# Kernel optimization log

Hardware: AMD Instinct MI355X
Metric: run time of the kernel (lower is better)

## Reference

```python
import jax, jax.numpy as jnp
import numpy as np

G = 250          # grid_size hardcoded in forward
CENTER = G // 2  # 125
K = 1000         # max steps of torch.linspace(r, 2, int((2-r)*500)+1) for r in (0,1)
PAD = 1          # kernel_size // 2 for kernel_size=3
PRED = 10


def rasterize(lidar):
    """Vectorized polar_to_cartesian: lidar [B,360] -> binary grid [B,1,G,G]."""
    B = lidar.shape[0]
    dtype = lidar.dtype
    angles = jnp.linspace(0.0, 2.0 * jnp.pi, 360)            # [360]
    r = lidar                                                 # [B,360]
    valid_r = (r > 0.0) & (r < 1.0)
    # steps = int((2-r)*500) + 1  (positive -> floor == trunc)
    n = jnp.floor((2.0 - r) * 500.0).astype(jnp.int32) + 1   # [B,360], in [501,1000]
    k = jnp.arange(K, dtype=jnp.int32)                        # [K]
    denom = jnp.maximum(n - 1, 1).astype(dtype)
    # torch.linspace(r, 2, n): mag_k = r + k*(2-r)/(n-1)
    mag = r[..., None] + k.astype(dtype) * (2.0 - r)[..., None] / denom[..., None]  # [B,360,K]
    step_ok = k[None, None, :] < n[..., None]
    x = mag * jnp.cos(angles)[None, :, None]
    y = mag * jnp.sin(angles)[None, :, None]
    # int(.) truncates toward zero
    xg = jnp.trunc(CENTER + x * 100.0).astype(jnp.int32)
    yg = jnp.trunc(CENTER + y * 100.0).astype(jnp.int32)
    inb = (xg >= 0) & (xg < G) & (yg >= 0) & (yg < G)
    valid = valid_r[..., None] & step_ok & inb               # [B,360,K]
    idx = jnp.where(valid, yg * G + xg, G * G)               # invalid -> sentinel slot
    flat = jnp.zeros((B, G * G + 1), dtype=dtype)
    flat = flat.at[jnp.arange(B)[:, None, None], idx].max(valid.astype(dtype))
    return flat[:, : G * G].reshape(B, 1, G, G)


def conv2d(x, w, b):
    y = jax.lax.conv_general_dilated(
        x, w, window_strides=(1, 1), padding=[(PAD, PAD), (PAD, PAD)],
        dimension_numbers=("NCHW", "OIHW", "NCHW"))
    return y + b[None, :, None, None]


def linear(x, w, b):  # torch convention: w [out,in]
    return x @ w.T + b


def setup_inputs() -> dict:
    key = jax.random.key(0)
    ks = jax.random.split(key, 18)
    B = 8
    HW, HL = 64, 64  # hidden_size_wind, hidden_size_lidar
    conv_out = 32 * G * G  # 2,000,000

    def w(k, shape, fan_in):
        return jax.random.normal(k, shape, dtype=jnp.float32) / np.float32(np.sqrt(fan_in))

    return {
        "lidar": jax.random.uniform(ks[0], (B, 360), dtype=jnp.float32),
        "wind": jax.random.normal(ks[1], (B, 2), dtype=jnp.float32),
        "w_wind1": w(ks[2], (HW, 2), 2), "b_wind1": jnp.zeros((HW,), jnp.float32),
        "w_wind2": w(ks[3], (HW, HW), HW), "b_wind2": jnp.zeros((HW,), jnp.float32),
        "w_wind3": w(ks[4], (HW, HW), HW), "b_wind3": jnp.zeros((HW,), jnp.float32),
        "conv1_w": w(ks[5], (16, 1, 3, 3), 9), "conv1_b": jnp.zeros((16,), jnp.float32),
        "conv2_w": w(ks[6], (32, 16, 3, 3), 16 * 9), "conv2_b": jnp.zeros((32,), jnp.float32),
        "fc1_w": w(ks[7], (HL, conv_out + HW), conv_out + HW), "fc1_b": jnp.zeros((HL,), jnp.float32),
        "fc2_w": w(ks[8], (HL // 2, HL), HL), "fc2_b": jnp.zeros((HL // 2,), jnp.float32),
        "fc3_w": w(ks[9], (2 * PRED * PRED, HL // 2), HL // 2), "fc3_b": jnp.zeros((2 * PRED * PRED,), jnp.float32),
    }


def reference(lidar, wind, w_wind1, b_wind1, w_wind2, b_wind2, w_wind3, b_wind3,
              conv1_w, conv1_b, conv2_w, conv2_b, fc1_w, fc1_b, fc2_w, fc2_b, fc3_w, fc3_b):
    B = lidar.shape[0]
    img = rasterize(lidar)                                    # [B,1,250,250]
    wnd = jax.nn.relu(linear(wind, w_wind1, b_wind1))
    wnd = jax.nn.relu(linear(wnd, w_wind2, b_wind2))
    wnd = jax.nn.relu(linear(wnd, w_wind3, b_wind3))          # [B,64]
    h = jax.nn.relu(conv2d(img, conv1_w, conv1_b))            # [B,16,250,250]
    h = jax.nn.relu(conv2d(h, conv2_w, conv2_b))              # [B,32,250,250]
    h = h.reshape(B, -1)                                      # [B,2000000]
    x = jnp.concatenate([h, wnd], axis=1)
    x = jax.nn.relu(linear(x, fc1_w, fc1_b))
    x = jax.nn.relu(linear(x, fc2_w, fc2_b))
    x = linear(x, fc3_w, fc3_b)
    return x.reshape(B, PRED, PRED, 2)
```

## Files before the change

### kernel.cpp

```cpp
#include <hip/hip_runtime.h>

#define G 250
#define GG 62500
#define NB 8
#define HFEAT 2000000
#define W1STRIDE 2000064

__global__ void k_raster(const float* __restrict__ lidar, float* __restrict__ img) {
    int idx = blockIdx.x * blockDim.x + threadIdx.x;
    if (idx >= NB * 360 * 1000) return;
    int k = idx % 1000;
    int ba = idx / 1000;
    int a = ba % 360;
    int b = ba / 360;
    float r = lidar[ba];
    if (!(r > 0.0f && r < 1.0f)) return;
    float tmr = __fsub_rn(2.0f, r);
    int n = (int)floorf(__fmul_rn(tmr, 500.0f)) + 1;
    if (k >= n) return;
    float denom = (float)(n - 1);
    const float delta = 6.2831855f / 359.0f;
    float angle = __fmul_rn((float)a, delta);
    float mag = __fadd_rn(r, __fdiv_rn(__fmul_rn((float)k, tmr), denom));
    float c = cosf(angle);
    float s = sinf(angle);
    float px = __fadd_rn(125.0f, __fmul_rn(__fmul_rn(mag, c), 100.0f));
    float py = __fadd_rn(125.0f, __fmul_rn(__fmul_rn(mag, s), 100.0f));
    int xg = (int)px;
    int yg = (int)py;
    if (xg >= 0 && xg < G && yg >= 0 && yg < G)
        img[b * GG + yg * G + xg] = 1.0f;
}

__global__ void k_conv1(const float* __restrict__ img, const float* __restrict__ w,
                        const float* __restrict__ bias, float* __restrict__ c1) {
    __shared__ float sw[144];
    __shared__ float sb[16];
    int t = threadIdx.x;
    if (t < 144) sw[t] = w[t];
    if (t < 16) sb[t] = bias[t];
    __syncthreads();
    int p = blockIdx.x * 256 + t;
    if (p >= NB * GG) return;
    int b = p / GG;
    int yx = p - b * GG;
    int y = yx / G;
    int x = yx - y * G;
    float in[9];
#pragma unroll
    for (int dy = 0; dy < 3; ++dy)
#pragma unroll
        for (int dx = 0; dx < 3; ++dx) {
            int gy = y + dy - 1, gx = x + dx - 1;
            in[dy * 3 + dx] = (gy >= 0 && gy < G && gx >= 0 && gx < G)
                                  ? img[b * GG + gy * G + gx] : 0.0f;
        }
#pragma unroll
    for (int co = 0; co < 16; ++co) {
        float a = sb[co];
#pragma unroll
        for (int k = 0; k < 9; ++k) a = fmaf(in[k], sw[co * 9 + k], a);
        c1[(b * 16 + co) * GG + yx] = fmaxf(a, 0.0f);
    }
}

__global__ __launch_bounds__(256) void k_conv2(const float* __restrict__ c1,
                                               const float* __restrict__ w,
                                               const float* __restrict__ bias,
                                               float* __restrict__ h) {
    __shared__ float s_in[16][18][35];
    __shared__ float s_w[4608];
    int t = threadIdx.x;
    int bx = blockIdx.x, by = blockIdx.y, b = blockIdx.z;
    for (int i = t; i < 4608; i += 256) s_w[i] = w[i];
    int x0 = bx * 32 - 1, y0 = by * 16 - 1;
    for (int i = t; i < 16 * 18 * 34; i += 256) {
        int ci = i / (18 * 34);
        int rem = i - ci * (18 * 34);
        int yy = rem / 34;
        int xx = rem - yy * 34;
        int gy = y0 + yy, gx = x0 + xx;
        float v = 0.0f;
        if (gy >= 0 && gy < G && gx >= 0 && gx < G)
            v = c1[(b * 16 + ci) * GG + gy * G + gx];
        s_in[ci][yy][xx] = v;
    }
    __syncthreads();
    int pg = t & 63;
    int cog = t >> 6;
    int ry = pg >> 2;
    int rx = (pg & 3) * 8;
    float acc[8][8];
#pragma unroll
    for (int i = 0; i < 8; ++i)
#pragma unroll
        for (int j = 0; j < 8; ++j) acc[i][j] = 0.0f;
    for (int ci = 0; ci < 16; ++ci) {
        float in[3][10];
#pragma unroll
        for (int dy = 0; dy < 3; ++dy)
#pragma unroll
            for (int xx = 0; xx < 10; ++xx)
                in[dy][xx] = s_in[ci][ry + dy][rx + xx];
#pragma unroll
        for (int coi = 0; coi < 8; ++coi) {
            const float* wp = &s_w[(cog * 8 + coi) * 144 + ci * 9];
            float w0 = wp[0], w1 = wp[1], w2 = wp[2], w3 = wp[3], w4 = wp[4],
                  w5 = wp[5], w6 = wp[6], w7 = wp[7], w8 = wp[8];
#pragma unroll
            for (int px = 0; px < 8; ++px) {
                float a = acc[coi][px];
                a = fmaf(in[0][px],     w0, a);
                a = fmaf(in[0][px + 1], w1, a);
                a = fmaf(in[0][px + 2], w2, a);
                a = fmaf(in[1][px],     w3, a);
                a = fmaf(in[1][px + 1], w4, a);
                a = fmaf(in[1][px + 2], w5, a);
                a = fmaf(in[2][px],     w6, a);
                a = fmaf(in[2][px + 1], w7, a);
                a = fmaf(in[2][px + 2], w8, a);
                acc[coi][px] = a;
            }
        }
    }
    int y = by * 16 + ry;
    if (y < G) {
#pragma unroll
        for (int coi = 0; coi < 8; ++coi) {
            int co = cog * 8 + coi;
            float bv = bias[co];
#pragma unroll
            for (int px = 0; px < 8; ++px) {
                int x = bx * 32 + rx + px;
                if (x < G)
                    h[((size_t)(b * 32 + co)) * GG + y * G + x] =
                        fmaxf(acc[coi][px] + bv, 0.0f);
            }
        }
    }
}

__global__ __launch_bounds__(512) void k_fc1(const float* __restrict__ h,
                                             const float* __restrict__ W1,
                                             float* __restrict__ accout) {
    int t = threadIdx.x;
    int w = t >> 6;
    int l = t & 63;
    int gw = blockIdx.x * 8 + w;
    int g = gw & 7;
    int c0 = gw >> 3;
    float acc[64];
#pragma unroll
    for (int i = 0; i < 64; ++i) acc[i] = 0.0f;
    const int NCH = (HFEAT + 255) / 256;
    for (int c = c0; c < NCH; c += 512) {
        int j = c * 256 + l * 4;
        if (j < HFEAT) {
            float4 hv[8];
#pragma unroll
            for (int b = 0; b < 8; ++b)
                hv[b] = *(const float4*)(h + (size_t)b * HFEAT + j);
#pragma unroll
            for (int oi = 0; oi < 8; ++oi) {
                int o = g * 8 + oi;
                float4 wv = *(const float4*)(W1 + (size_t)o * W1STRIDE + j);
#pragma unroll
                for (int b = 0; b < 8; ++b) {
                    float a = acc[oi * 8 + b];
                    a = fmaf(wv.x, hv[b].x, a);
                    a = fmaf(wv.y, hv[b].y, a);
                    a = fmaf(wv.z, hv[b].z, a);
                    a = fmaf(wv.w, hv[b].w, a);
                    acc[oi * 8 + b] = a;
                }
            }
        }
    }
    int cnt = 64;
#pragma unroll
    for (int s = 0; s < 6; ++s) {
        int half = cnt >> 1;
        bool up = (l >> s) & 1;
#pragma unroll
        for (int i = 0; i < half; ++i) {
            float send = up ? acc[i] : acc[i + half];
            float keep = up ? acc[i + half] : acc[i];
            float recv = __shfl_xor(send, 1 << s, 64);
            acc[i] = keep + recv;
        }
        cnt = half;
    }
    unsigned vi = __brev((unsigned)l) >> 26;
    atomicAdd(&accout[g * 64 + vi], acc[0]);
}

__global__ void k_final(const float* __restrict__ wind,
                        const float* __restrict__ ww1, const float* __restrict__ wb1,
                        const float* __restrict__ ww2, const float* __restrict__ wb2,
                        const float* __restrict__ ww3, const float* __restrict__ wb3,
                        const float* __restrict__ W1, const float* __restrict__ fb1,
                        const float* __restrict__ acc,
                        const float* __restrict__ w2, const float* __restrict__ b2,
                        const float* __restrict__ w3, const float* __restrict__ b3,
                        float* __restrict__ out) {
    __shared__ float s1[8][64], s2[8][64], f1[8][64], f2[8][32];
    int t = threadIdx.x;
    if (t < 64) {
        for (int b = 0; b < 8; ++b) {
            float v = wb1[t] + ww1[t * 2] * wind[b * 2] + ww1[t * 2 + 1] * wind[b * 2 + 1];
            s1[b][t] = fmaxf(v, 0.0f);
        }
    }
    __syncthreads();
    if (t < 64) {
        for (int b = 0; b < 8; ++b) {
            float v = wb2[t];
            for (int k = 0; k < 64; ++k) v = fmaf(s1[b][k], ww2[t * 64 + k], v);
            s2[b][t] = fmaxf(v, 0.0f);
        }
    }
    __syncthreads();
    if (t < 64) {
        for (int b = 0; b < 8; ++b) {
            float v = wb3[t];
            for (int k = 0; k < 64; ++k) v = fmaf(s2[b][k], ww3[t * 64 + k], v);
            s1[b][t] = fmaxf(v, 0.0f);
        }
    }
    __syncthreads();
    if (t < 64) {
        for (int b = 0; b < 8; ++b) {
            float v = fb1[t] + acc[t * 8 + b];
            const float* wrow = W1 + (size_t)t * W1STRIDE + HFEAT;
            for (int k = 0; k < 64; ++k) v = fmaf(s1[b][k], wrow[k], v);
            f1[b][t] = fmaxf(v, 0.0f);
        }
    }
    __syncthreads();
    if (t < 32) {
        for (int b = 0; b < 8; ++b) {
            float v = b2[t];
            for (int k = 0; k < 64; ++k) v = fmaf(f1[b][k], w2[t * 64 + k], v);
            f2[b][t] = fmaxf(v, 0.0f);
        }
    }
    __syncthreads();
    if (t < 200) {
        for (int b = 0; b < 8; ++b) {
            float v = b3[t];
            for (int k = 0; k < 32; ++k) v = fmaf(f2[b][k], w3[t * 32 + k], v);
            out[b * 200 + t] = v;
        }
    }
}

extern "C" void kernel_launch(void* const* d_in, const int* in_sizes, int n_in,
                              void* d_out, int out_size, void* d_ws, size_t ws_size,
                              hipStream_t stream) {
    const float* lidar = (const float*)d_in[0];
    const float* wind  = (const float*)d_in[1];
    const float* ww1 = (const float*)d_in[2];
    const float* wb1 = (const float*)d_in[3];
    const float* ww2 = (const float*)d_in[4];
    const float* wb2 = (const float*)d_in[5];
    const float* ww3 = (const float*)d_in[6];
    const float* wb3 = (const float*)d_in[7];
    const float* c1w = (const float*)d_in[8];
    const float* c1b = (const float*)d_in[9];
    const float* c2w = (const float*)d_in[10];
    const float* c2b = (const float*)d_in[11];
    const float* fw1 = (const float*)d_in[12];
    const float* fb1 = (const float*)d_in[13];
    const float* fw2 = (const float*)d_in[14];
    const float* fb2 = (const float*)d_in[15];
    const float* fw3 = (const float*)d_in[16];
    const float* fb3 = (const float*)d_in[17];
    float* out = (float*)d_out;

    float* ws  = (float*)d_ws;
    float* img = ws;
    float* c1  = ws + 500000;
    float* h   = ws + 8500000;
    float* acc = ws + 24500000;

    hipMemsetAsync(img, 0, 500000 * sizeof(float), stream);
    hipMemsetAsync(acc, 0, 512 * sizeof(float), stream);

    k_raster<<<(NB * 360 * 1000 + 255) / 256, 256, 0, stream>>>(lidar, img);
    k_conv1<<<(NB * GG + 255) / 256, 256, 0, stream>>>(img, c1w, c1b, c1);
    dim3 g2(8, 16, NB);
    k_conv2<<<g2, 256, 0, stream>>>(c1, c2w, c2b, h);
    k_fc1<<<512, 512, 0, stream>>>(h, fw1, acc);
    k_final<<<1, 256, 0, stream>>>(wind, ww1, wb1, ww2, wb2, ww3, wb3,
                                   fw1, fb1, acc, fw2, fb2, fw3, fb3, out);
}
```

Measured before the change: 274.9 us.

## Fuse conv1 into conv2 tile and restructure fc1 block shape and loads

Conv1 is now computed per tile in shared memory from a haloed image tile inside the conv2 kernel, so the 16-channel intermediate is no longer written to and re-read from global memory, and one launch is removed. Halo pixels of conv1 are recomputed per tile. Separately, fc1 moves from 512-thread to 256-thread blocks (doubling the grid) with a min-blocks launch bound, and all eight weight float4 loads are issued before the FMAs to expose more memory-level parallelism. This raises register pressure.

```diff
diff --git a/kernel.cpp b/kernel.cpp
--- a/kernel.cpp
+++ b/kernel.cpp
@@ -32,58 +32,48 @@
         img[b * GG + yg * G + xg] = 1.0f;
 }
 
-__global__ void k_conv1(const float* __restrict__ img, const float* __restrict__ w,
-                        const float* __restrict__ bias, float* __restrict__ c1) {
-    __shared__ float sw[144];
-    __shared__ float sb[16];
-    int t = threadIdx.x;
-    if (t < 144) sw[t] = w[t];
-    if (t < 16) sb[t] = bias[t];
-    __syncthreads();
-    int p = blockIdx.x * 256 + t;
-    if (p >= NB * GG) return;
-    int b = p / GG;
-    int yx = p - b * GG;
-    int y = yx / G;
-    int x = yx - y * G;
-    float in[9];
-#pragma unroll
-    for (int dy = 0; dy < 3; ++dy)
-#pragma unroll
-        for (int dx = 0; dx < 3; ++dx) {
-            int gy = y + dy - 1, gx = x + dx - 1;
-            in[dy * 3 + dx] = (gy >= 0 && gy < G && gx >= 0 && gx < G)
-                                  ? img[b * GG + gy * G + gx] : 0.0f;
-        }
-#pragma unroll
-    for (int co = 0; co < 16; ++co) {
-        float a = sb[co];
-#pragma unroll
-        for (int k = 0; k < 9; ++k) a = fmaf(in[k], sw[co * 9 + k], a);
-        c1[(b * 16 + co) * GG + yx] = fmaxf(a, 0.0f);
-    }
-}
-
-__global__ __launch_bounds__(256) void k_conv2(const float* __restrict__ c1,
-                                               const float* __restrict__ w,
-                                               const float* __restrict__ bias,
-                                               float* __restrict__ h) {
-    __shared__ float s_in[16][18][35];
-    __shared__ float s_w[4608];
+__global__ __launch_bounds__(256) void k_conv12(const float* __restrict__ img,
+                                                const float* __restrict__ w1,
+                                                const float* __restrict__ b1,
+                                                const float* __restrict__ w2,
+                                                const float* __restrict__ b2,
+                                                float* __restrict__ h) {
+    __shared__ float s_img[20][37];
+    __shared__ float s_c1[16][18][35];
+    __shared__ float s_w2[4608];
+    __shared__ float s_w1[144];
+    __shared__ float s_b1[16];
     int t = threadIdx.x;
     int bx = blockIdx.x, by = blockIdx.y, b = blockIdx.z;
-    for (int i = t; i < 4608; i += 256) s_w[i] = w[i];
+    for (int i = t; i < 4608; i += 256) s_w2[i] = w2[i];
+    if (t < 144) s_w1[t] = w1[t];
+    if (t < 16) s_b1[t] = b1[t];
     int x0 = bx * 32 - 1, y0 = by * 16 - 1;
-    for (int i = t; i < 16 * 18 * 34; i += 256) {
-        int ci = i / (18 * 34);
-        int rem = i - ci * (18 * 34);
-        int yy = rem / 34;
-        int xx = rem - yy * 34;
+    for (int i = t; i < 20 * 36; i += 256) {
+        int r = i / 36, c = i - r * 36;
+        int gy = y0 - 1 + r, gx = x0 - 1 + c;
+        float v = 0.0f;
+        if (gy >= 0 && gy < G && gx >= 0 && gx < G) v = img[b * GG + gy * G + gx];
+        s_img[r][c] = v;
+    }
+    __syncthreads();
+    for (int i = t; i < 612; i += 256) {
+        int yy = i / 34, xx = i - yy * 34;
         int gy = y0 + yy, gx = x0 + xx;
-        float v = 0.0f;
-        if (gy >= 0 && gy < G && gx >= 0 && gx < G)
-            v = c1[(b * 16 + ci) * GG + gy * G + gx];
-        s_in[ci][yy][xx] = v;
+        bool inb = (gy >= 0 && gy < G && gx >= 0 && gx < G);
+        float iv[9];
+#pragma unroll
+        for (int dy = 0; dy < 3; ++dy)
+#pragma unroll
+            for (int dx = 0; dx < 3; ++dx)
+                iv[dy * 3 + dx] = s_img[yy + dy][xx + dx];
+#pragma unroll
+        for (int co = 0; co < 16; ++co) {
+            float a = s_b1[co];
+#pragma unroll
+            for (int k = 0; k < 9; ++k) a = fmaf(iv[k], s_w1[co * 9 + k], a);
+            s_c1[co][yy][xx] = inb ? fmaxf(a, 0.0f) : 0.0f;
+        }
     }
     __syncthreads();
     int pg = t & 63;
@@ -101,24 +91,24 @@
         for (int dy = 0; dy < 3; ++dy)
 #pragma unroll
             for (int xx = 0; xx < 10; ++xx)
-                in[dy][xx] = s_in[ci][ry + dy][rx + xx];
+                in[dy][xx] = s_c1[ci][ry + dy][rx + xx];
 #pragma unroll
         for (int coi = 0; coi < 8; ++coi) {
-            const float* wp = &s_w[(cog * 8 + coi) * 144 + ci * 9];
-            float w0 = wp[0], w1 = wp[1], w2 = wp[2], w3 = wp[3], w4 = wp[4],
+            const float* wp = &s_w2[(cog * 8 + coi) * 144 + ci * 9];
+            float w0 = wp[0], w1v = wp[1], w2v = wp[2], w3 = wp[3], w4 = wp[4],
                   w5 = wp[5], w6 = wp[6], w7 = wp[7], w8 = wp[8];
 #pragma unroll
             for (int px = 0; px < 8; ++px) {
                 float a = acc[coi][px];
-                a = fmaf(in[0][px],     w0, a);
-                a = fmaf(in[0][px + 1], w1, a);
-                a = fmaf(in[0][px + 2], w2, a);
-                a = fmaf(in[1][px],     w3, a);
-                a = fmaf(in[1][px + 1], w4, a);
-                a = fmaf(in[1][px + 2], w5, a);
-                a = fmaf(in[2][px],     w6, a);
-                a = fmaf(in[2][px + 1], w7, a);
-                a = fmaf(in[2][px + 2], w8, a);
+                a = fmaf(in[0][px],     w0,  a);
+                a = fmaf(in[0][px + 1], w1v, a);
+                a = fmaf(in[0][px + 2], w2v, a);
+                a = fmaf(in[1][px],     w3,  a);
+                a = fmaf(in[1][px + 1], w4,  a);
+                a = fmaf(in[1][px + 2], w5,  a);
+                a = fmaf(in[2][px],     w6,  a);
+                a = fmaf(in[2][px + 1], w7,  a);
+                a = fmaf(in[2][px + 2], w8,  a);
                 acc[coi][px] = a;
             }
         }
@@ -128,7 +118,7 @@
 #pragma unroll
         for (int coi = 0; coi < 8; ++coi) {
             int co = cog * 8 + coi;
-            float bv = bias[co];
+            float bv = b2[co];
 #pragma unroll
             for (int px = 0; px < 8; ++px) {
                 int x = bx * 32 + rx + px;
@@ -140,13 +130,13 @@
     }
 }
 
-__global__ __launch_bounds__(512) void k_fc1(const float* __restrict__ h,
-                                             const float* __restrict__ W1,
-                                             float* __restrict__ accout) {
+__global__ __launch_bounds__(256, 3) void k_fc1(const float* __restrict__ h,
+                                                const float* __restrict__ W1,
+                                                float* __restrict__ accout) {
     int t = threadIdx.x;
     int w = t >> 6;
     int l = t & 63;
-    int gw = blockIdx.x * 8 + w;
+    int gw = blockIdx.x * 4 + w;
     int g = gw & 7;
     int c0 = gw >> 3;
     float acc[64];
@@ -156,21 +146,22 @@
     for (int c = c0; c < NCH; c += 512) {
         int j = c * 256 + l * 4;
         if (j < HFEAT) {
-            float4 hv[8];
+            float4 hv[8], wv[8];
 #pragma unroll
             for (int b = 0; b < 8; ++b)
                 hv[b] = *(const float4*)(h + (size_t)b * HFEAT + j);
 #pragma unroll
+            for (int oi = 0; oi < 8; ++oi)
+                wv[oi] = *(const float4*)(W1 + (size_t)(g * 8 + oi) * W1STRIDE + j);
+#pragma unroll
             for (int oi = 0; oi < 8; ++oi) {
-                int o = g * 8 + oi;
-                float4 wv = *(const float4*)(W1 + (size_t)o * W1STRIDE + j);
 #pragma unroll
                 for (int b = 0; b < 8; ++b) {
                     float a = acc[oi * 8 + b];
-                    a = fmaf(wv.x, hv[b].x, a);
-                    a = fmaf(wv.y, hv[b].y, a);
-                    a = fmaf(wv.z, hv[b].z, a);
-                    a = fmaf(wv.w, hv[b].w, a);
+                    a = fmaf(wv[oi].x, hv[b].x, a);
+                    a = fmaf(wv[oi].y, hv[b].y, a);
+                    a = fmaf(wv[oi].z, hv[b].z, a);
+                    a = fmaf(wv[oi].w, hv[b].w, a);
                     acc[oi * 8 + b] = a;
                 }
             }
@@ -279,18 +270,16 @@
 
     float* ws  = (float*)d_ws;
     float* img = ws;
-    float* c1  = ws + 500000;
-    float* h   = ws + 8500000;
-    float* acc = ws + 24500000;
+    float* h   = ws + 500000;
+    float* acc = ws + 16500000;
 
     hipMemsetAsync(img, 0, 500000 * sizeof(float), stream);
     hipMemsetAsync(acc, 0, 512 * sizeof(float), stream);
 
     k_raster<<<(NB * 360 * 1000 + 255) / 256, 256, 0, stream>>>(lidar, img);
-    k_conv1<<<(NB * GG + 255) / 256, 256, 0, stream>>>(img, c1w, c1b, c1);
     dim3 g2(8, 16, NB);
-    k_conv2<<<g2, 256, 0, stream>>>(c1, c2w, c2b, h);
-    k_fc1<<<512, 512, 0, stream>>>(h, fw1, acc);
+    k_conv12<<<g2, 256, 0, stream>>>(img, c1w, c1b, c2w, c2b, h);
+    k_fc1<<<1024, 256, 0, stream>>>(h, fw1, acc);
     k_final<<<1, 256, 0, stream>>>(wind, ww1, wb1, ww2, wb2, ww3, wb3,
                                    fw1, fb1, acc, fw2, fb2, fw3, fb3, out);
 }
```

New measurement: 269.5 us. 2.0% less time.
